# Performance work log

Measured on AMD Instinct MI355X. Metric: run time of the kernel, lower is better.

The kernel has to match this reference:

```python
import jax, jax.numpy as jnp
import numpy as np

DT = 1.0          # ODENet default dt
W_SCALE = 0.05    # keep forward-Euler trajectory numerically tame


def setup_inputs() -> dict:
    key = jax.random.key(0)
    ks = jax.random.split(key, 4)
    T, B, H = 8192, 128, 128
    x = jax.random.normal(ks[0], (T, B, 1), dtype=jnp.float32)
    W1 = jax.random.normal(ks[1], (2, H), dtype=jnp.float32) * W_SCALE
    b1 = jnp.zeros((H,), dtype=jnp.float32)
    W2 = jax.random.normal(ks[2], (H, H), dtype=jnp.float32) * W_SCALE
    b2 = jnp.zeros((H,), dtype=jnp.float32)
    W3 = jax.random.normal(ks[3], (H, 1), dtype=jnp.float32) * W_SCALE
    b3 = jnp.zeros((1,), dtype=jnp.float32)
    return {"x": x, "W1": W1, "b1": b1, "W2": W2, "b2": b2, "W3": W3, "b3": b3}


def reference(x, W1, b1, W2, b2, W3, b3):
    # x: (T, B, 1). State y: (B,), init zeros (initial_value in ODENet.forward).
    # Forward Euler: y_{n+1} = y_n + dt * f(x_n, y_n), returning all T states
    # (y_0 included), i.e. output shape (T, B, 1) matching the input shape.
    x_sq = x[..., 0]                      # (T, B) == self.derivative_network.input
    B = x_sq.shape[1]
    y0 = jnp.zeros((B,), dtype=x.dtype)   # initial_value

    def deriv(xt, y):
        inp = jnp.stack([xt, y], axis=-1)          # (B, 2)
        h = jnp.tanh(inp @ W1 + b1)                # (B, H)
        h = jnp.tanh(h @ W2 + b2)                  # (B, H)
        return (h @ W3 + b3)[..., 0]               # (B,)

    def step(y, xt):
        y_next = y + DT * deriv(xt, y)
        return y_next, y_next

    # T-1 Euler steps produce states y_1..y_{T-1}
    _, ys = jax.lax.scan(step, y0, x_sq[:-1])      # (T-1, B)
    out = jnp.concatenate([y0[None], ys], axis=0)  # (T, B)
    return out[..., None]                          # (T, B, 1)
```

## Files before the change

### kernel.cpp

```cpp
#include <hip/hip_runtime.h>

#define T_STEPS 8192
#define BATCH   128
#define HID     128
#define NTHR    256

typedef float v2f __attribute__((ext_vector_type(2)));

__device__ __forceinline__ float fast_tanh(float z) {
    float e = __expf(2.0f * z);
    float r = __builtin_amdgcn_rcpf(1.0f + e);
    return fmaf(-2.0f, r, 1.0f);
}

__device__ __forceinline__ float pair_sum(float x) {
    int t1 = __builtin_amdgcn_update_dpp(0, __builtin_bit_cast(int, x),
                                         0xB1 ,
                                         0xf, 0xf, false);
    return x + __builtin_bit_cast(float, t1);
}

__device__ __forceinline__ float wave_sum_pairuniform_l63(float x) {
#define DPP_ADD(ctrl) do {                                                        \
        int t_ = __builtin_amdgcn_update_dpp(0, __builtin_bit_cast(int, x),       \
                                             (ctrl), 0xf, 0xf, false);            \
        x += __builtin_bit_cast(float, t_); } while (0)
    DPP_ADD(0x112);
    DPP_ADD(0x114);
    DPP_ADD(0x118);
    DPP_ADD(0x142);
    DPP_ADD(0x143);
#undef DPP_ADD
    return x;
}

__device__ __forceinline__ float bcast_lane(float v, int l) {
    int r = __builtin_amdgcn_readlane(__builtin_bit_cast(int, v), l);
    return __builtin_bit_cast(float, r);
}

#define FORALL32(M) M(0) M(1) M(2) M(3) M(4) M(5) M(6) M(7) \
                    M(8) M(9) M(10) M(11) M(12) M(13) M(14) M(15) \
                    M(16) M(17) M(18) M(19) M(20) M(21) M(22) M(23) \
                    M(24) M(25) M(26) M(27) M(28) M(29) M(30) M(31)

__global__ __launch_bounds__(NTHR, 2) void odenet_scan(
    const float* __restrict__ x,
    const float* __restrict__ W1, const float* __restrict__ b1,
    const float* __restrict__ W2, const float* __restrict__ b2,
    const float* __restrict__ W3, const float* __restrict__ b3,
    float* __restrict__ out) {

    const int b    = blockIdx.x;
    const int tid  = threadIdx.x;
    const int w    = tid >> 6;
    const int lane = tid & 63;
    const int j    = (w << 5) | (lane >> 1);
    const int s    = lane & 1;

    __shared__ __align__(16) float h1buf[4][136];
    __shared__ __align__(16) float dyx[2][4];

    const float* col = W2 + j;
    const int kb = s << 6;
#define DECLW(i) v2f wp##i = {col[(kb + 2*(i) + 0) * HID],                        \
                              col[(kb + 2*(i) + 1) * HID]};
    FORALL32(DECLW)
#undef DECLW
#define PINW(i) asm volatile("" : "+v"(wp##i));
    FORALL32(PINW)
#undef PINW

    float w1xa = W1[lane],      w1ya = W1[HID + lane],      b1a = b1[lane];
    float w1xb = W1[lane + 64], w1yb = W1[HID + lane + 64], b1b = b1[lane + 64];
    float b2j = b2[j], w3j = W3[j], b3v = b3[0];
    asm volatile("" : "+v"(w1xa), "+v"(w1ya), "+v"(b1a),
                      "+v"(w1xb), "+v"(w1yb), "+v"(b1b),
                      "+v"(b2j), "+v"(w3j), "+v"(b3v));

    float y    = 0.0f;
    float ybuf = 0.0f;
    if (w == 0 && lane == 0) out[b] = 0.0f;

    float xbuf  = x[lane * BATCH + b];
    int   nb    = 64;
    float xnext = x[min(nb + lane, T_STEPS - 1) * BATCH + b];
    float xv = bcast_lane(xbuf, 0);
    float ax = fmaf(xv, w1xa, b1a);
    float bx = fmaf(xv, w1xb, b1b);

    const float4* h4 = (const float4*)&h1buf[w][s * 68];

    for (int t = 0; t < T_STEPS - 1; ++t) {
        const int tm = t & 63;

        float ha = fast_tanh(fmaf(y, w1ya, ax));
        float hb = fast_tanh(fmaf(y, w1yb, bx));
        h1buf[w][lane]      = ha;
        h1buf[w][68 + lane] = hb;

        v2f a0 = {0.f, 0.f}, a1 = {0.f, 0.f}, a2 = {0.f, 0.f}, a3 = {0.f, 0.f};
        {
            float4 q;
#define FMAP(qi, WA, WB, AA, AB) q = h4[qi];                                      \
            { v2f lo = {q.x, q.y}, hi = {q.z, q.w};                               \
              AA += WA * lo; AB += WB * hi; }
            FMAP( 0, wp0 , wp1 , a0, a1) FMAP( 1, wp2 , wp3 , a2, a3)
            FMAP( 2, wp4 , wp5 , a0, a1) FMAP( 3, wp6 , wp7 , a2, a3)
            FMAP( 4, wp8 , wp9 , a0, a1) FMAP( 5, wp10, wp11, a2, a3)
            FMAP( 6, wp12, wp13, a0, a1) FMAP( 7, wp14, wp15, a2, a3)
            FMAP( 8, wp16, wp17, a0, a1) FMAP( 9, wp18, wp19, a2, a3)
            FMAP(10, wp20, wp21, a0, a1) FMAP(11, wp22, wp23, a2, a3)
            FMAP(12, wp24, wp25, a0, a1) FMAP(13, wp26, wp27, a2, a3)
            FMAP(14, wp28, wp29, a0, a1) FMAP(15, wp30, wp31, a2, a3)
#undef FMAP
        }
        v2f ap = (a0 + a1) + (a2 + a3);

        float z2  = pair_sum(ap.x + ap.y);
        float h2  = fast_tanh(z2 + b2j);
        float dyw = wave_sum_pairuniform_l63(w3j * h2);
        if (lane == 63) dyx[t & 1][w] = dyw;

        const int tmn = (t + 1) & 63;
        if (tmn == 0) {
            xbuf = xnext;
            nb += 64;
            xnext = x[min(nb + lane, T_STEPS - 1) * BATCH + b];
        }
        float xvn = bcast_lane(xbuf, tmn);
        float axn = fmaf(xvn, w1xa, b1a);
        float bxn = fmaf(xvn, w1xb, b1b);

        asm volatile("s_waitcnt lgkmcnt(0)\n\ts_barrier" ::: "memory");

        float4 d = *(const float4*)&dyx[t & 1][0];
        y += ((d.x + d.y) + (d.z + d.w)) + b3v;

        ybuf = (lane == tm) ? y : ybuf;
        if (w == 0 && tm == 63)
            out[(t - 62 + lane) * BATCH + b] = ybuf;

        ax = axn; bx = bxn;
    }
    if (w == 0 && lane < 63)
        out[(T_STEPS - 63 + lane) * BATCH + b] = ybuf;
}

extern "C" void kernel_launch(void* const* d_in, const int* in_sizes, int n_in,
                              void* d_out, int out_size, void* d_ws, size_t ws_size,
                              hipStream_t stream) {
    const float* x  = (const float*)d_in[0];
    const float* W1 = (const float*)d_in[1];
    const float* b1 = (const float*)d_in[2];
    const float* W2 = (const float*)d_in[3];
    const float* b2 = (const float*)d_in[4];
    const float* W3 = (const float*)d_in[5];
    const float* b3 = (const float*)d_in[6];

    odenet_scan<<<dim3(BATCH), dim3(NTHR), 0, stream>>>(
        x, W1, b1, W2, b2, W3, b3, (float*)d_out);
}
```

Measured before the change: 4.015 ms.

## Process two batch elements per block to interleave independent recurrences

Each block now advances two batch elements' Euler recurrences in lockstep, sharing the register-resident W2 columns and a single barrier per step. The grid is halved to 64 blocks. The aim is to hide the serial latency chain (tanh, LDS dot, DPP reductions, barrier) by interleaving two independent dependency chains and amortising barrier cost. The trade-off is twice the per-step instruction work per block and fewer active CUs.

```diff
diff --git a/kernel.cpp b/kernel.cpp
--- a/kernel.cpp
+++ b/kernel.cpp
@@ -44,6 +44,23 @@
                     M(16) M(17) M(18) M(19) M(20) M(21) M(22) M(23) \
                     M(24) M(25) M(26) M(27) M(28) M(29) M(30) M(31)
 
+#define FMAP(H4, qi, WA, WB, AA, AB) {                                            \
+        float4 q_ = (H4)[qi];                                                     \
+        v2f lo_ = {q_.x, q_.y}, hi_ = {q_.z, q_.w};                               \
+        AA += (WA) * lo_; AB += (WB) * hi_; }
+
+#define L2DOT(H4, AP) do {                                                        \
+        v2f a0_={0.f,0.f}, a1_={0.f,0.f}, a2_={0.f,0.f}, a3_={0.f,0.f};           \
+        FMAP(H4, 0, wp0 , wp1 , a0_, a1_) FMAP(H4, 1, wp2 , wp3 , a2_, a3_)       \
+        FMAP(H4, 2, wp4 , wp5 , a0_, a1_) FMAP(H4, 3, wp6 , wp7 , a2_, a3_)       \
+        FMAP(H4, 4, wp8 , wp9 , a0_, a1_) FMAP(H4, 5, wp10, wp11, a2_, a3_)       \
+        FMAP(H4, 6, wp12, wp13, a0_, a1_) FMAP(H4, 7, wp14, wp15, a2_, a3_)       \
+        FMAP(H4, 8, wp16, wp17, a0_, a1_) FMAP(H4, 9, wp18, wp19, a2_, a3_)       \
+        FMAP(H4,10, wp20, wp21, a0_, a1_) FMAP(H4,11, wp22, wp23, a2_, a3_)       \
+        FMAP(H4,12, wp24, wp25, a0_, a1_) FMAP(H4,13, wp26, wp27, a2_, a3_)       \
+        FMAP(H4,14, wp28, wp29, a0_, a1_) FMAP(H4,15, wp30, wp31, a2_, a3_)       \
+        AP = (a0_ + a1_) + (a2_ + a3_); } while (0)
+
 __global__ __launch_bounds__(NTHR, 2) void odenet_scan(
     const float* __restrict__ x,
     const float* __restrict__ W1, const float* __restrict__ b1,
@@ -51,15 +68,16 @@
     const float* __restrict__ W3, const float* __restrict__ b3,
     float* __restrict__ out) {
 
-    const int b    = blockIdx.x;
+    const int be0  = blockIdx.x * 2;
+    const int be1  = be0 + 1;
     const int tid  = threadIdx.x;
     const int w    = tid >> 6;
     const int lane = tid & 63;
     const int j    = (w << 5) | (lane >> 1);
     const int s    = lane & 1;
 
-    __shared__ __align__(16) float h1buf[4][136];
-    __shared__ __align__(16) float dyx[2][4];
+    __shared__ __align__(16) float h1buf[2][4][136];
+    __shared__ __align__(16) float dyx[2][2][4];
 
     const float* col = W2 + j;
     const int kb = s << 6;
@@ -78,73 +96,89 @@
                       "+v"(w1xb), "+v"(w1yb), "+v"(b1b),
                       "+v"(b2j), "+v"(w3j), "+v"(b3v));
 
-    float y    = 0.0f;
-    float ybuf = 0.0f;
-    if (w == 0 && lane == 0) out[b] = 0.0f;
+    float y0 = 0.0f, y1 = 0.0f;
+    float ybuf0 = 0.0f, ybuf1 = 0.0f;
+    if (w == 0 && lane == 0) { out[be0] = 0.0f; out[be1] = 0.0f; }
 
-    float xbuf  = x[lane * BATCH + b];
+    float xbuf0 = x[lane * BATCH + be0];
+    float xbuf1 = x[lane * BATCH + be1];
     int   nb    = 64;
-    float xnext = x[min(nb + lane, T_STEPS - 1) * BATCH + b];
-    float xv = bcast_lane(xbuf, 0);
-    float ax = fmaf(xv, w1xa, b1a);
-    float bx = fmaf(xv, w1xb, b1b);
+    float xnext0 = x[min(nb + lane, T_STEPS - 1) * BATCH + be0];
+    float xnext1 = x[min(nb + lane, T_STEPS - 1) * BATCH + be1];
+    float xv0 = bcast_lane(xbuf0, 0);
+    float xv1 = bcast_lane(xbuf1, 0);
+    float ax0 = fmaf(xv0, w1xa, b1a);
+    float bx0 = fmaf(xv0, w1xb, b1b);
+    float ax1 = fmaf(xv1, w1xa, b1a);
+    float bx1 = fmaf(xv1, w1xb, b1b);
 
-    const float4* h4 = (const float4*)&h1buf[w][s * 68];
+    const float4* h40 = (const float4*)&h1buf[0][w][s * 68];
+    const float4* h41 = (const float4*)&h1buf[1][w][s * 68];
 
     for (int t = 0; t < T_STEPS - 1; ++t) {
         const int tm = t & 63;
+        const int p  = t & 1;
 
-        float ha = fast_tanh(fmaf(y, w1ya, ax));
-        float hb = fast_tanh(fmaf(y, w1yb, bx));
-        h1buf[w][lane]      = ha;
-        h1buf[w][68 + lane] = hb;
+        float ha0 = fast_tanh(fmaf(y0, w1ya, ax0));
+        float hb0 = fast_tanh(fmaf(y0, w1yb, bx0));
+        h1buf[0][w][lane]      = ha0;
+        h1buf[0][w][68 + lane] = hb0;
+        float ha1 = fast_tanh(fmaf(y1, w1ya, ax1));
+        float hb1 = fast_tanh(fmaf(y1, w1yb, bx1));
+        h1buf[1][w][lane]      = ha1;
+        h1buf[1][w][68 + lane] = hb1;
 
-        v2f a0 = {0.f, 0.f}, a1 = {0.f, 0.f}, a2 = {0.f, 0.f}, a3 = {0.f, 0.f};
-        {
-            float4 q;
-#define FMAP(qi, WA, WB, AA, AB) q = h4[qi];                                      \
-            { v2f lo = {q.x, q.y}, hi = {q.z, q.w};                               \
-              AA += WA * lo; AB += WB * hi; }
-            FMAP( 0, wp0 , wp1 , a0, a1) FMAP( 1, wp2 , wp3 , a2, a3)
-            FMAP( 2, wp4 , wp5 , a0, a1) FMAP( 3, wp6 , wp7 , a2, a3)
-            FMAP( 4, wp8 , wp9 , a0, a1) FMAP( 5, wp10, wp11, a2, a3)
-            FMAP( 6, wp12, wp13, a0, a1) FMAP( 7, wp14, wp15, a2, a3)
-            FMAP( 8, wp16, wp17, a0, a1) FMAP( 9, wp18, wp19, a2, a3)
-            FMAP(10, wp20, wp21, a0, a1) FMAP(11, wp22, wp23, a2, a3)
-            FMAP(12, wp24, wp25, a0, a1) FMAP(13, wp26, wp27, a2, a3)
-            FMAP(14, wp28, wp29, a0, a1) FMAP(15, wp30, wp31, a2, a3)
-#undef FMAP
-        }
-        v2f ap = (a0 + a1) + (a2 + a3);
+        v2f ap0;
+        L2DOT(h40, ap0);
+        float z20  = pair_sum(ap0.x + ap0.y);
+        float h20  = fast_tanh(z20 + b2j);
+        float dyw0 = wave_sum_pairuniform_l63(w3j * h20);
+        if (lane == 63) dyx[p][0][w] = dyw0;
 
-        float z2  = pair_sum(ap.x + ap.y);
-        float h2  = fast_tanh(z2 + b2j);
-        float dyw = wave_sum_pairuniform_l63(w3j * h2);
-        if (lane == 63) dyx[t & 1][w] = dyw;
+        v2f ap1;
+        L2DOT(h41, ap1);
+        float z21  = pair_sum(ap1.x + ap1.y);
+        float h21  = fast_tanh(z21 + b2j);
+        float dyw1 = wave_sum_pairuniform_l63(w3j * h21);
+        if (lane == 63) dyx[p][1][w] = dyw1;
 
         const int tmn = (t + 1) & 63;
         if (tmn == 0) {
-            xbuf = xnext;
+            xbuf0 = xnext0;
+            xbuf1 = xnext1;
             nb += 64;
-            xnext = x[min(nb + lane, T_STEPS - 1) * BATCH + b];
+            const int xi = min(nb + lane, T_STEPS - 1) * BATCH;
+            xnext0 = x[xi + be0];
+            xnext1 = x[xi + be1];
         }
-        float xvn = bcast_lane(xbuf, tmn);
-        float axn = fmaf(xvn, w1xa, b1a);
-        float bxn = fmaf(xvn, w1xb, b1b);
+        float xvn0 = bcast_lane(xbuf0, tmn);
+        float xvn1 = bcast_lane(xbuf1, tmn);
+        float axn0 = fmaf(xvn0, w1xa, b1a);
+        float bxn0 = fmaf(xvn0, w1xb, b1b);
+        float axn1 = fmaf(xvn1, w1xa, b1a);
+        float bxn1 = fmaf(xvn1, w1xb, b1b);
 
         asm volatile("s_waitcnt lgkmcnt(0)\n\ts_barrier" ::: "memory");
 
-        float4 d = *(const float4*)&dyx[t & 1][0];
-        y += ((d.x + d.y) + (d.z + d.w)) + b3v;
+        float4 d0 = *(const float4*)&dyx[p][0][0];
+        float4 d1 = *(const float4*)&dyx[p][1][0];
+        y0 += ((d0.x + d0.y) + (d0.z + d0.w)) + b3v;
+        y1 += ((d1.x + d1.y) + (d1.z + d1.w)) + b3v;
 
-        ybuf = (lane == tm) ? y : ybuf;
-        if (w == 0 && tm == 63)
-            out[(t - 62 + lane) * BATCH + b] = ybuf;
+        ybuf0 = (lane == tm) ? y0 : ybuf0;
+        ybuf1 = (lane == tm) ? y1 : ybuf1;
+        if (tm == 63) {
+            if (w == 0)      out[(t - 62 + lane) * BATCH + be0] = ybuf0;
+            else if (w == 1) out[(t - 62 + lane) * BATCH + be1] = ybuf1;
+        }
 
-        ax = axn; bx = bxn;
+        ax0 = axn0; bx0 = bxn0;
+        ax1 = axn1; bx1 = bxn1;
     }
-    if (w == 0 && lane < 63)
-        out[(T_STEPS - 63 + lane) * BATCH + b] = ybuf;
+    if (lane < 63) {
+        if (w == 0)      out[(T_STEPS - 63 + lane) * BATCH + be0] = ybuf0;
+        else if (w == 1) out[(T_STEPS - 63 + lane) * BATCH + be1] = ybuf1;
+    }
 }
 
 extern "C" void kernel_launch(void* const* d_in, const int* in_sizes, int n_in,
@@ -158,6 +192,6 @@
     const float* W3 = (const float*)d_in[5];
     const float* b3 = (const float*)d_in[6];
 
-    odenet_scan<<<dim3(BATCH), dim3(NTHR), 0, stream>>>(
+    odenet_scan<<<dim3(BATCH / 2), dim3(NTHR), 0, stream>>>(
         x, W1, b1, W2, b2, W3, b3, (float*)d_out);
 }
```

Measured after the change: 7.108 ms. +77.0%, slower.

## Split K across four lanes with two output columns per lane

Applied to the files above, without the earlier changes.

Each lane now computes partial dot products for two hidden columns over a 32-element K slice, instead of one column over 64 elements. This halves the LDS float4 reads per lane (8 instead of 16), since each loaded h1 vector feeds two columns. It adds a second DPP step to the partial-sum reduction and a second tanh per lane, and uses a shorter wave reduction afterwards. The LDS read pattern changes, so bank conflicts may differ from before.

```diff
diff --git a/kernel.cpp b/kernel.cpp
--- a/kernel.cpp
+++ b/kernel.cpp
@@ -13,19 +13,22 @@
     return fmaf(-2.0f, r, 1.0f);
 }
 
-__device__ __forceinline__ float pair_sum(float x) {
+__device__ __forceinline__ float quad_sum(float x) {
     int t1 = __builtin_amdgcn_update_dpp(0, __builtin_bit_cast(int, x),
                                          0xB1 ,
                                          0xf, 0xf, false);
-    return x + __builtin_bit_cast(float, t1);
+    x += __builtin_bit_cast(float, t1);
+    int t2 = __builtin_amdgcn_update_dpp(0, __builtin_bit_cast(int, x),
+                                         0x4E ,
+                                         0xf, 0xf, false);
+    return x + __builtin_bit_cast(float, t2);
 }
 
-__device__ __forceinline__ float wave_sum_pairuniform_l63(float x) {
+__device__ __forceinline__ float wave_sum_quaduniform_l63(float x) {
 #define DPP_ADD(ctrl) do {                                                        \
         int t_ = __builtin_amdgcn_update_dpp(0, __builtin_bit_cast(int, x),       \
                                              (ctrl), 0xf, 0xf, false);            \
         x += __builtin_bit_cast(float, t_); } while (0)
-    DPP_ADD(0x112);
     DPP_ADD(0x114);
     DPP_ADD(0x118);
     DPP_ADD(0x142);
@@ -39,10 +42,8 @@
     return __builtin_bit_cast(float, r);
 }
 
-#define FORALL32(M) M(0) M(1) M(2) M(3) M(4) M(5) M(6) M(7) \
-                    M(8) M(9) M(10) M(11) M(12) M(13) M(14) M(15) \
-                    M(16) M(17) M(18) M(19) M(20) M(21) M(22) M(23) \
-                    M(24) M(25) M(26) M(27) M(28) M(29) M(30) M(31)
+#define FORALL16(M) M(0) M(1) M(2) M(3) M(4) M(5) M(6) M(7) \
+                    M(8) M(9) M(10) M(11) M(12) M(13) M(14) M(15)
 
 __global__ __launch_bounds__(NTHR, 2) void odenet_scan(
     const float* __restrict__ x,
@@ -55,28 +56,34 @@
     const int tid  = threadIdx.x;
     const int w    = tid >> 6;
     const int lane = tid & 63;
-    const int j    = (w << 5) | (lane >> 1);
-    const int s    = lane & 1;
+    const int jg   = lane >> 2;
+    const int kc   = lane & 3;
+    const int j0   = (w << 5) | (jg << 1);
+    const int j1   = j0 + 1;
+    const int kb   = kc << 5;
 
     __shared__ __align__(16) float h1buf[4][136];
     __shared__ __align__(16) float dyx[2][4];
 
-    const float* col = W2 + j;
-    const int kb = s << 6;
-#define DECLW(i) v2f wp##i = {col[(kb + 2*(i) + 0) * HID],                        \
-                              col[(kb + 2*(i) + 1) * HID]};
-    FORALL32(DECLW)
+    const float* c0p = W2 + j0;
+    const float* c1p = W2 + j1;
+#define DECLW(i) v2f wp##i = {c0p[(kb + 2*(i) + 0) * HID],                        \
+                              c0p[(kb + 2*(i) + 1) * HID]};                       \
+                 v2f up##i = {c1p[(kb + 2*(i) + 0) * HID],                        \
+                              c1p[(kb + 2*(i) + 1) * HID]};
+    FORALL16(DECLW)
 #undef DECLW
-#define PINW(i) asm volatile("" : "+v"(wp##i));
-    FORALL32(PINW)
+#define PINW(i) asm volatile("" : "+v"(wp##i), "+v"(up##i));
+    FORALL16(PINW)
 #undef PINW
 
     float w1xa = W1[lane],      w1ya = W1[HID + lane],      b1a = b1[lane];
     float w1xb = W1[lane + 64], w1yb = W1[HID + lane + 64], b1b = b1[lane + 64];
-    float b2j = b2[j], w3j = W3[j], b3v = b3[0];
+    float b2j0 = b2[j0], b2j1 = b2[j1];
+    float w3j0 = W3[j0], w3j1 = W3[j1], b3v = b3[0];
     asm volatile("" : "+v"(w1xa), "+v"(w1ya), "+v"(b1a),
                       "+v"(w1xb), "+v"(w1yb), "+v"(b1b),
-                      "+v"(b2j), "+v"(w3j), "+v"(b3v));
+                      "+v"(b2j0), "+v"(b2j1), "+v"(w3j0), "+v"(w3j1), "+v"(b3v));
 
     float y    = 0.0f;
     float ybuf = 0.0f;
@@ -89,7 +96,8 @@
     float ax = fmaf(xv, w1xa, b1a);
     float bx = fmaf(xv, w1xb, b1b);
 
-    const float4* h4 = (const float4*)&h1buf[w][s * 68];
+    const float4* h4 = (const float4*)((const char*)&h1buf[w][0] +
+                                       ((kc >> 1) * 272 + (kc & 1) * 128));
 
     for (int t = 0; t < T_STEPS - 1; ++t) {
         const int tm = t & 63;
@@ -99,27 +107,29 @@
         h1buf[w][lane]      = ha;
         h1buf[w][68 + lane] = hb;
 
-        v2f a0 = {0.f, 0.f}, a1 = {0.f, 0.f}, a2 = {0.f, 0.f}, a3 = {0.f, 0.f};
+        v2f a0 = {0.f, 0.f}, a1 = {0.f, 0.f};
+        v2f c0 = {0.f, 0.f}, c1 = {0.f, 0.f};
         {
             float4 q;
-#define FMAP(qi, WA, WB, AA, AB) q = h4[qi];                                      \
+#define FMAP(qi, WA, WB, UA, UB) q = h4[qi];                                      \
             { v2f lo = {q.x, q.y}, hi = {q.z, q.w};                               \
-              AA += WA * lo; AB += WB * hi; }
-            FMAP( 0, wp0 , wp1 , a0, a1) FMAP( 1, wp2 , wp3 , a2, a3)
-            FMAP( 2, wp4 , wp5 , a0, a1) FMAP( 3, wp6 , wp7 , a2, a3)
-            FMAP( 4, wp8 , wp9 , a0, a1) FMAP( 5, wp10, wp11, a2, a3)
-            FMAP( 6, wp12, wp13, a0, a1) FMAP( 7, wp14, wp15, a2, a3)
-            FMAP( 8, wp16, wp17, a0, a1) FMAP( 9, wp18, wp19, a2, a3)
-            FMAP(10, wp20, wp21, a0, a1) FMAP(11, wp22, wp23, a2, a3)
-            FMAP(12, wp24, wp25, a0, a1) FMAP(13, wp26, wp27, a2, a3)
-            FMAP(14, wp28, wp29, a0, a1) FMAP(15, wp30, wp31, a2, a3)
+              a0 += WA * lo; a1 += WB * hi;                                       \
+              c0 += UA * lo; c1 += UB * hi; }
+            FMAP(0, wp0 , wp1 , up0 , up1 ) FMAP(1, wp2 , wp3 , up2 , up3 )
+            FMAP(2, wp4 , wp5 , up4 , up5 ) FMAP(3, wp6 , wp7 , up6 , up7 )
+            FMAP(4, wp8 , wp9 , up8 , up9 ) FMAP(5, wp10, wp11, up10, up11)
+            FMAP(6, wp12, wp13, up12, up13) FMAP(7, wp14, wp15, up14, up15)
 #undef FMAP
         }
-        v2f ap = (a0 + a1) + (a2 + a3);
+        v2f as_ = a0 + a1;
+        v2f cs_ = c0 + c1;
 
-        float z2  = pair_sum(ap.x + ap.y);
-        float h2  = fast_tanh(z2 + b2j);
-        float dyw = wave_sum_pairuniform_l63(w3j * h2);
+        float z0 = quad_sum(as_.x + as_.y);
+        float z1 = quad_sum(cs_.x + cs_.y);
+        float h20 = fast_tanh(z0 + b2j0);
+        float h21 = fast_tanh(z1 + b2j1);
+        float dyv = fmaf(w3j0, h20, w3j1 * h21);
+        float dyw = wave_sum_quaduniform_l63(dyv);
         if (lane == 63) dyx[t & 1][w] = dyw;
 
         const int tmn = (t + 1) & 63;
```

Measured after the change: 3.557 ms. -11.4%, faster.

## Collapse each batch row onto a single wavefront, dropping the cross-wave barrier

Applied to the files above, without the earlier changes.

Each batch element now runs on one 64-lane wavefront instead of four. Every lane owns two W2 columns, with half the weights pinned in VGPRs and half in AGPRs. The per-step s_barrier and the LDS exchange of partial dy values are replaced by a full in-wave DPP reduction and a readlane broadcast. The aim is to remove barrier and cross-wave sync latency from the serial recurrence, at the cost of twice the FMA work per lane per step. It also depends on AGPR operands feeding the packed FMAs, which may need extra accvgpr read instructions.

```diff
diff --git a/kernel.cpp b/kernel.cpp
--- a/kernel.cpp
+++ b/kernel.cpp
@@ -3,7 +3,7 @@
 #define T_STEPS 8192
 #define BATCH   128
 #define HID     128
-#define NTHR    256
+#define NTHR    64
 
 typedef float v2f __attribute__((ext_vector_type(2)));
 
@@ -13,18 +13,12 @@
     return fmaf(-2.0f, r, 1.0f);
 }
 
-__device__ __forceinline__ float pair_sum(float x) {
-    int t1 = __builtin_amdgcn_update_dpp(0, __builtin_bit_cast(int, x),
-                                         0xB1 ,
-                                         0xf, 0xf, false);
-    return x + __builtin_bit_cast(float, t1);
-}
-
-__device__ __forceinline__ float wave_sum_pairuniform_l63(float x) {
+__device__ __forceinline__ float wave_sum_l63(float x) {
 #define DPP_ADD(ctrl) do {                                                        \
         int t_ = __builtin_amdgcn_update_dpp(0, __builtin_bit_cast(int, x),       \
                                              (ctrl), 0xf, 0xf, false);            \
         x += __builtin_bit_cast(float, t_); } while (0)
+    DPP_ADD(0x111);
     DPP_ADD(0x112);
     DPP_ADD(0x114);
     DPP_ADD(0x118);
@@ -39,12 +33,16 @@
     return __builtin_bit_cast(float, r);
 }
 
-#define FORALL32(M) M(0) M(1) M(2) M(3) M(4) M(5) M(6) M(7) \
-                    M(8) M(9) M(10) M(11) M(12) M(13) M(14) M(15) \
-                    M(16) M(17) M(18) M(19) M(20) M(21) M(22) M(23) \
-                    M(24) M(25) M(26) M(27) M(28) M(29) M(30) M(31)
+#define FORALL64(M) M(0) M(1) M(2) M(3) M(4) M(5) M(6) M(7) \
+    M(8) M(9) M(10) M(11) M(12) M(13) M(14) M(15) \
+    M(16) M(17) M(18) M(19) M(20) M(21) M(22) M(23) \
+    M(24) M(25) M(26) M(27) M(28) M(29) M(30) M(31) \
+    M(32) M(33) M(34) M(35) M(36) M(37) M(38) M(39) \
+    M(40) M(41) M(42) M(43) M(44) M(45) M(46) M(47) \
+    M(48) M(49) M(50) M(51) M(52) M(53) M(54) M(55) \
+    M(56) M(57) M(58) M(59) M(60) M(61) M(62) M(63)
 
-__global__ __launch_bounds__(NTHR, 2) void odenet_scan(
+__global__ __launch_bounds__(NTHR, 1) void odenet_scan(
     const float* __restrict__ x,
     const float* __restrict__ W1, const float* __restrict__ b1,
     const float* __restrict__ W2, const float* __restrict__ b2,
@@ -52,35 +50,38 @@
     float* __restrict__ out) {
 
     const int b    = blockIdx.x;
-    const int tid  = threadIdx.x;
-    const int w    = tid >> 6;
-    const int lane = tid & 63;
-    const int j    = (w << 5) | (lane >> 1);
-    const int s    = lane & 1;
+    const int lane = threadIdx.x;
+    const int jA   = lane;
+    const int jB   = lane + 64;
 
-    __shared__ __align__(16) float h1buf[4][136];
-    __shared__ __align__(16) float dyx[2][4];
+    __shared__ __align__(16) float h1buf[128];
 
-    const float* col = W2 + j;
-    const int kb = s << 6;
-#define DECLW(i) v2f wp##i = {col[(kb + 2*(i) + 0) * HID],                        \
-                              col[(kb + 2*(i) + 1) * HID]};
-    FORALL32(DECLW)
-#undef DECLW
-#define PINW(i) asm volatile("" : "+v"(wp##i));
-    FORALL32(PINW)
-#undef PINW
+    const float* cA = W2 + jA;
+    const float* cB = W2 + jB;
+#define DECLA(i) v2f wa##i = {cA[(2*(i)    ) * HID], cA[(2*(i) + 1) * HID]};
+#define DECLB(i) v2f wb##i = {cB[(2*(i)    ) * HID], cB[(2*(i) + 1) * HID]};
+    FORALL64(DECLA)
+    FORALL64(DECLB)
+#undef DECLA
+#undef DECLB
+#define PINA(i) asm volatile("" : "+v"(wa##i));
+#define PINB(i) asm volatile("" : "+a"(wb##i));
+    FORALL64(PINA)
+    FORALL64(PINB)
+#undef PINA
+#undef PINB
 
     float w1xa = W1[lane],      w1ya = W1[HID + lane],      b1a = b1[lane];
     float w1xb = W1[lane + 64], w1yb = W1[HID + lane + 64], b1b = b1[lane + 64];
-    float b2j = b2[j], w3j = W3[j], b3v = b3[0];
+    float b2A = b2[jA], b2B = b2[jB];
+    float w3A = W3[jA], w3B = W3[jB], b3v = b3[0];
     asm volatile("" : "+v"(w1xa), "+v"(w1ya), "+v"(b1a),
                       "+v"(w1xb), "+v"(w1yb), "+v"(b1b),
-                      "+v"(b2j), "+v"(w3j), "+v"(b3v));
+                      "+v"(b2A), "+v"(b2B), "+v"(w3A), "+v"(w3B), "+v"(b3v));
 
     float y    = 0.0f;
     float ybuf = 0.0f;
-    if (w == 0 && lane == 0) out[b] = 0.0f;
+    if (lane == 0) out[b] = 0.0f;
 
     float xbuf  = x[lane * BATCH + b];
     int   nb    = 64;
@@ -89,38 +90,44 @@
     float ax = fmaf(xv, w1xa, b1a);
     float bx = fmaf(xv, w1xb, b1b);
 
-    const float4* h4 = (const float4*)&h1buf[w][s * 68];
+    const float4* h4 = (const float4*)h1buf;
 
     for (int t = 0; t < T_STEPS - 1; ++t) {
         const int tm = t & 63;
 
         float ha = fast_tanh(fmaf(y, w1ya, ax));
         float hb = fast_tanh(fmaf(y, w1yb, bx));
-        h1buf[w][lane]      = ha;
-        h1buf[w][68 + lane] = hb;
+        h1buf[lane]      = ha;
+        h1buf[64 + lane] = hb;
 
-        v2f a0 = {0.f, 0.f}, a1 = {0.f, 0.f}, a2 = {0.f, 0.f}, a3 = {0.f, 0.f};
+        v2f a0 = {0.f, 0.f}, a1 = {0.f, 0.f};
+        v2f c0 = {0.f, 0.f}, c1 = {0.f, 0.f};
         {
             float4 q;
-#define FMAP(qi, WA, WB, AA, AB) q = h4[qi];                                      \
+#define FM(qi, A0, A1, B0, B1) q = h4[qi];                                        \
             { v2f lo = {q.x, q.y}, hi = {q.z, q.w};                               \
-              AA += WA * lo; AB += WB * hi; }
-            FMAP( 0, wp0 , wp1 , a0, a1) FMAP( 1, wp2 , wp3 , a2, a3)
-            FMAP( 2, wp4 , wp5 , a0, a1) FMAP( 3, wp6 , wp7 , a2, a3)
-            FMAP( 4, wp8 , wp9 , a0, a1) FMAP( 5, wp10, wp11, a2, a3)
-            FMAP( 6, wp12, wp13, a0, a1) FMAP( 7, wp14, wp15, a2, a3)
-            FMAP( 8, wp16, wp17, a0, a1) FMAP( 9, wp18, wp19, a2, a3)
-            FMAP(10, wp20, wp21, a0, a1) FMAP(11, wp22, wp23, a2, a3)
-            FMAP(12, wp24, wp25, a0, a1) FMAP(13, wp26, wp27, a2, a3)
-            FMAP(14, wp28, wp29, a0, a1) FMAP(15, wp30, wp31, a2, a3)
-#undef FMAP
+              a0 += A0 * lo; a1 += A1 * hi;                                       \
+              c0 += B0 * lo; c1 += B1 * hi; }
+            FM( 0, wa0 , wa1 , wb0 , wb1 ) FM( 1, wa2 , wa3 , wb2 , wb3 )
+            FM( 2, wa4 , wa5 , wb4 , wb5 ) FM( 3, wa6 , wa7 , wb6 , wb7 )
+            FM( 4, wa8 , wa9 , wb8 , wb9 ) FM( 5, wa10, wa11, wb10, wb11)
+            FM( 6, wa12, wa13, wb12, wb13) FM( 7, wa14, wa15, wb14, wb15)
+            FM( 8, wa16, wa17, wb16, wb17) FM( 9, wa18, wa19, wb18, wb19)
+            FM(10, wa20, wa21, wb20, wb21) FM(11, wa22, wa23, wb22, wb23)
+            FM(12, wa24, wa25, wb24, wb25) FM(13, wa26, wa27, wb26, wb27)
+            FM(14, wa28, wa29, wb28, wb29) FM(15, wa30, wa31, wb30, wb31)
+            FM(16, wa32, wa33, wb32, wb33) FM(17, wa34, wa35, wb34, wb35)
+            FM(18, wa36, wa37, wb36, wb37) FM(19, wa38, wa39, wb38, wb39)
+            FM(20, wa40, wa41, wb40, wb41) FM(21, wa42, wa43, wb42, wb43)
+            FM(22, wa44, wa45, wb44, wb45) FM(23, wa46, wa47, wb46, wb47)
+            FM(24, wa48, wa49, wb48, wb49) FM(25, wa50, wa51, wb50, wb51)
+            FM(26, wa52, wa53, wb52, wb53) FM(27, wa54, wa55, wb54, wb55)
+            FM(28, wa56, wa57, wb56, wb57) FM(29, wa58, wa59, wb58, wb59)
+            FM(30, wa60, wa61, wb60, wb61) FM(31, wa62, wa63, wb62, wb63)
+#undef FM
         }
-        v2f ap = (a0 + a1) + (a2 + a3);
-
-        float z2  = pair_sum(ap.x + ap.y);
-        float h2  = fast_tanh(z2 + b2j);
-        float dyw = wave_sum_pairuniform_l63(w3j * h2);
-        if (lane == 63) dyx[t & 1][w] = dyw;
+        v2f as_ = a0 + a1;
+        v2f cs_ = c0 + c1;
 
         const int tmn = (t + 1) & 63;
         if (tmn == 0) {
@@ -132,18 +139,21 @@
         float axn = fmaf(xvn, w1xa, b1a);
         float bxn = fmaf(xvn, w1xb, b1b);
 
-        asm volatile("s_waitcnt lgkmcnt(0)\n\ts_barrier" ::: "memory");
+        float h2A = fast_tanh((as_.x + as_.y) + b2A);
+        float h2B = fast_tanh((cs_.x + cs_.y) + b2B);
+        float dyv = fmaf(w3A, h2A, w3B * h2B);
+        float dyw = wave_sum_l63(dyv);
+        float dy  = bcast_lane(dyw, 63);
 
-        float4 d = *(const float4*)&dyx[t & 1][0];
-        y += ((d.x + d.y) + (d.z + d.w)) + b3v;
+        y += dy + b3v;
 
         ybuf = (lane == tm) ? y : ybuf;
-        if (w == 0 && tm == 63)
+        if (tm == 63)
             out[(t - 62 + lane) * BATCH + b] = ybuf;
 
         ax = axn; bx = bxn;
     }
-    if (w == 0 && lane < 63)
+    if (lane < 63)
         out[(T_STEPS - 63 + lane) * BATCH + b] = ybuf;
 }
 
```

After: 7.050 ms. +75.6%, slower.
